# Kernel optimization log

Measured on AMD Instinct MI355X. Metric: run time of the kernel, lower is better.

Reference implementation:

```python
import jax, jax.numpy as jnp
import numpy as np
from jax import lax

K1, K2, DATA_RANGE = 0.01, 0.03, 1.0
MS_WEIGHTS = np.array([0.0448, 0.2856, 0.3001, 0.2363, 0.1333], dtype=np.float32)


def _gauss1d(size, sigma):
    coords = jnp.arange(size, dtype=jnp.float32) - size // 2
    g = jnp.exp(-(coords ** 2) / (2.0 * sigma ** 2))
    return g / jnp.sum(g)


def _gaussian_blur(x, win1d):
    # separable depthwise gaussian blur, VALID padding (matches pytorch-msssim)
    C = x.shape[1]
    size = win1d.shape[0]
    kh = jnp.tile(win1d.reshape(1, 1, size, 1), (C, 1, 1, 1))  # (C,1,k,1)
    kw = jnp.tile(win1d.reshape(1, 1, 1, size), (C, 1, 1, 1))  # (C,1,1,k)
    dn = ('NCHW', 'OIHW', 'NCHW')
    x = lax.conv_general_dilated(x, kh, (1, 1), 'VALID',
                                 dimension_numbers=dn, feature_group_count=C)
    x = lax.conv_general_dilated(x, kw, (1, 1), 'VALID',
                                 dimension_numbers=dn, feature_group_count=C)
    return x


def _ssim_per_channel(X, Y, win1d):
    C1 = (K1 * DATA_RANGE) ** 2
    C2 = (K2 * DATA_RANGE) ** 2
    mu1 = _gaussian_blur(X, win1d)
    mu2 = _gaussian_blur(Y, win1d)
    mu1_sq, mu2_sq, mu1_mu2 = mu1 * mu1, mu2 * mu2, mu1 * mu2
    sigma1_sq = _gaussian_blur(X * X, win1d) - mu1_sq
    sigma2_sq = _gaussian_blur(Y * Y, win1d) - mu2_sq
    sigma12 = _gaussian_blur(X * Y, win1d) - mu1_mu2
    cs_map = (2.0 * sigma12 + C2) / (sigma1_sq + sigma2_sq + C2)
    ssim_map = ((2.0 * mu1_mu2 + C1) / (mu1_sq + mu2_sq + C1)) * cs_map
    return ssim_map.mean(axis=(2, 3)), cs_map.mean(axis=(2, 3))  # (B,C) each


def _avg_pool2(x, ph, pw):
    # F.avg_pool2d(kernel=2, stride=2, padding=(ph,pw), count_include_pad=True)
    s = lax.reduce_window(x, 0.0, lax.add, (1, 1, 2, 2), (1, 1, 2, 2),
                          ((0, 0), (0, 0), (ph, ph), (pw, pw)))
    return s * 0.25


def _ms_ssim(gen, gt):
    weights = jnp.asarray(MS_WEIGHTS)
    win_size = 3 if gen.shape[3] < 256 else 11
    win1d = _gauss1d(win_size, 1.5)
    levels = weights.shape[0]
    mcs = []
    for i in range(levels):
        ssim_pc, cs = _ssim_per_channel(gen, gt, win1d)
        if i < levels - 1:
            mcs.append(jax.nn.relu(cs))
            ph, pw = gen.shape[2] % 2, gen.shape[3] % 2
            gen = _avg_pool2(gen, ph, pw)
            gt = _avg_pool2(gt, ph, pw)
    ssim_pc = jax.nn.relu(ssim_pc)
    mcs_and_ssim = jnp.stack(mcs + [ssim_pc], axis=0)  # (levels,B,C)
    ms_ssim_val = jnp.prod(mcs_and_ssim ** weights[:, None, None], axis=0)
    return ms_ssim_val.mean()


def setup_inputs() -> dict:
    key = jax.random.key(0)
    k1, k2 = jax.random.split(key)
    gen_frames = jax.random.uniform(k1, (16, 3, 512, 512), dtype=jnp.float32)
    gt_frames = jax.random.uniform(k2, (16, 3, 512, 512), dtype=jnp.float32)
    return {"gen_frames": gen_frames, "gt_frames": gt_frames}


def reference(gen_frames, gt_frames):
    return 1.0 - _ms_ssim(gen_frames, gt_frames)
```

## Files before the change

kernel.cpp:

```cpp
#include <hip/hip_runtime.h>


#define TW 32
#define TH 64
#define RPT 8
#define HALO 10
#define IW (TW + HALO)
#define IH (TH + HALO)
#define ISTR (IW + 1)

__device__ __constant__ float G11[11] = {
    0.001028380f, 0.007598758f, 0.036000773f, 0.109360680f, 0.213005529f,
    0.266011731f,
    0.213005529f, 0.109360680f, 0.036000773f, 0.007598758f, 0.001028380f
};

__device__ __forceinline__ float fastdiv(float a, float b) {
    float r = __builtin_amdgcn_rcpf(b);
    r = r * __builtin_fmaf(-b, r, 2.0f);
    return a * r;
}

#define HBLUR(ROW, SLOT) do {                                              \
    const float2* pxy_ = &sxy[(ROW) * ISTR + tx];                          \
    float bx_ = 0.f, by_ = 0.f, bxx_ = 0.f, byy_ = 0.f, bxy_ = 0.f;        \
    _Pragma("unroll")                                                      \
    for (int t_ = 0; t_ < 11; ++t_) {                                      \
        float w_  = G11[t_];                                               \
        float2 v_ = pxy_[t_];                                              \
        float wx_ = w_ * v_.x;                                             \
        float wy_ = w_ * v_.y;                                             \
        bx_  += wx_;                                                       \
        by_  += wy_;                                                       \
        bxx_ = __builtin_fmaf(wx_, v_.x, bxx_);                            \
        byy_ = __builtin_fmaf(wy_, v_.y, byy_);                            \
        bxy_ = __builtin_fmaf(wx_, v_.y, bxy_);                            \
    }                                                                      \
    rbx[(SLOT)] = bx_; rby[(SLOT)] = by_; rbxx[(SLOT)] = bxx_;             \
    rbyy[(SLOT)] = byy_; rbxy[(SLOT)] = bxy_;                              \
} while (0)

#define VTAP(I, T) do {                                                    \
    const float w_ = G11[(T)];                                             \
    m1  = __builtin_fmaf(w_, rbx [((I)+(T)) % 11], m1);                    \
    m2  = __builtin_fmaf(w_, rby [((I)+(T)) % 11], m2);                    \
    qxx = __builtin_fmaf(w_, rbxx[((I)+(T)) % 11], qxx);                   \
    qyy = __builtin_fmaf(w_, rbyy[((I)+(T)) % 11], qyy);                   \
    qxy = __builtin_fmaf(w_, rbxy[((I)+(T)) % 11], qxy);                   \
} while (0)

#define STEP(I) do {                                                       \
    HBLUR(g0 + 10 + (I), (10 + (I)) % 11);                                 \
    float m1 = 0.f, m2 = 0.f, qxx = 0.f, qyy = 0.f, qxy = 0.f;             \
    VTAP(I,0); VTAP(I,1); VTAP(I,2); VTAP(I,3); VTAP(I,4); VTAP(I,5);      \
    VTAP(I,6); VTAP(I,7); VTAP(I,8); VTAP(I,9); VTAP(I,10);                \
    if (colok && (oy + g0 + (I)) < Hs) {                                   \
        const float C1 = 0.0001f, C2 = 0.0009f;                            \
        float mu1s = m1 * m1, mu2s = m2 * m2, mu12 = m1 * m2;              \
        float s1  = qxx - mu1s;                                            \
        float s2  = qyy - mu2s;                                            \
        float s12 = qxy - mu12;                                            \
        float cs  = fastdiv(2.f * s12 + C2, s1 + s2 + C2);                 \
        float ss  = fastdiv((2.f * mu12 + C1) * cs, mu1s + mu2s + C1);     \
        ssum += ss;                                                        \
        csum += cs;                                                        \
    }                                                                      \
} while (0)

__global__ __launch_bounds__(256)
void ssim_level_kernel(const float* __restrict__ X, const float* __restrict__ Y,
                       int H, int W, int Hs, int Ws, float* __restrict__ acc,
                       float* __restrict__ Xo, float* __restrict__ Yo,
                       int Wp, int do_pool)
{
    __shared__ float2 sxy[IH * ISTR];
    __shared__ float red[2][4];

    const int bc  = blockIdx.z;
    const int ox  = blockIdx.x * TW;
    const int oy  = blockIdx.y * TH;
    const int tid = threadIdx.x;
    const size_t base = (size_t)bc * H * W;

    for (int p = tid; p < IH * 21; p += 256) {
        int r  = p / 21;
        int c2 = p - r * 21;
        int gr = oy + r;      if (gr > H - 1) gr = H - 1;
        int gc = ox + 2 * c2; if (gc > W - 2) gc = W - 2;
        size_t g = base + (size_t)gr * W + gc;
        float2 xv = *reinterpret_cast<const float2*>(X + g);
        float2 yv = *reinterpret_cast<const float2*>(Y + g);
        float2* dst = &sxy[r * ISTR + 2 * c2];
        dst[0] = make_float2(xv.x, yv.x);
        dst[1] = make_float2(xv.y, yv.y);
    }
    __syncthreads();

    const int tx = tid & 31;
    const int ty = tid >> 5;
    const int g0 = ty * RPT;

    float rbx[11], rby[11], rbxx[11], rbyy[11], rbxy[11];

    HBLUR(g0 + 0, 0); HBLUR(g0 + 1, 1); HBLUR(g0 + 2, 2); HBLUR(g0 + 3, 3);
    HBLUR(g0 + 4, 4); HBLUR(g0 + 5, 5); HBLUR(g0 + 6, 6); HBLUR(g0 + 7, 7);
    HBLUR(g0 + 8, 8); HBLUR(g0 + 9, 9);

    const bool colok = (ox + tx) < Ws;
    float ssum = 0.f, csum = 0.f;

    STEP(0); STEP(1); STEP(2); STEP(3);
    STEP(4); STEP(5); STEP(6); STEP(7);

    if (do_pool) {
        int i  = tid >> 3;
        int j0 = (tid & 7) * 2;
        const float2* r0 = &sxy[(2 * i)     * ISTR + 2 * j0];
        const float2* r1 = &sxy[(2 * i + 1) * ISTR + 2 * j0];
        float2 a0 = r0[0], a1 = r0[1], b0 = r1[0], b1 = r1[1];
        float2 c0 = r0[2], c1 = r0[3], d0 = r1[2], d1 = r1[3];
        float2 xo, yo;
        xo.x = 0.25f * (a0.x + a1.x + b0.x + b1.x);
        yo.x = 0.25f * (a0.y + a1.y + b0.y + b1.y);
        xo.y = 0.25f * (c0.x + c1.x + d0.x + d1.x);
        yo.y = 0.25f * (c0.y + c1.y + d0.y + d1.y);
        size_t po = (size_t)bc * Wp * Wp + (size_t)((oy >> 1) + i) * Wp + (ox >> 1) + j0;
        *reinterpret_cast<float2*>(Xo + po) = xo;
        *reinterpret_cast<float2*>(Yo + po) = yo;
    }

#pragma unroll
    for (int off = 32; off; off >>= 1) {
        ssum += __shfl_down(ssum, off);
        csum += __shfl_down(csum, off);
    }
    if ((tid & 63) == 0) {
        red[0][tid >> 6] = ssum;
        red[1][tid >> 6] = csum;
    }
    __syncthreads();
    if (tid == 0) {
        float s = red[0][0] + red[0][1] + red[0][2] + red[0][3];
        float c = red[1][0] + red[1][1] + red[1][2] + red[1][3];
        atomicAdd(&acc[bc * 2 + 0], s);
        atomicAdd(&acc[bc * 2 + 1], c);
    }
}

__launch_bounds__(64)
__global__ void finalize_kernel(const float* __restrict__ acc, float* __restrict__ out)
{
    const int lane = threadIdx.x;
    float prod = 0.f;
    if (lane < 48) {
        const float npix[5] = {252004.f, 60516.f, 13924.f, 2916.f, 484.f};
        const float wgt[5]  = {0.0448f, 0.2856f, 0.3001f, 0.2363f, 0.1333f};
        prod = 1.f;
#pragma unroll
        for (int l = 0; l < 5; ++l) {
            float v = (l < 4) ? acc[l * 96 + lane * 2 + 1] : acc[l * 96 + lane * 2 + 0];
            v = v / npix[l];
            v = fmaxf(v, 0.f);
            prod *= powf(v, wgt[l]);
        }
    }
#pragma unroll
    for (int off = 32; off; off >>= 1) prod += __shfl_down(prod, off);
    if (lane == 0) out[0] = 1.f - prod / 48.f;
}

extern "C" void kernel_launch(void* const* d_in, const int* in_sizes, int n_in,
                              void* d_out, int out_size, void* d_ws, size_t ws_size,
                              hipStream_t stream)
{
    const float* gen = (const float*)d_in[0];
    const float* gt  = (const float*)d_in[1];
    float* out = (float*)d_out;

    char* ws = (char*)d_ws;
    float* acc = (float*)ws;
    float* p   = (float*)(ws + 2048);
    float* g1 = p; p += (size_t)48 * 256 * 256;
    float* t1 = p; p += (size_t)48 * 256 * 256;
    float* g2 = p; p += (size_t)48 * 128 * 128;
    float* t2 = p; p += (size_t)48 * 128 * 128;
    float* g3 = p; p += (size_t)48 * 64 * 64;
    float* t3 = p; p += (size_t)48 * 64 * 64;
    float* g4 = p; p += (size_t)48 * 32 * 32;
    float* t4 = p; p += (size_t)48 * 32 * 32;

    hipMemsetAsync(acc, 0, 5 * 48 * 2 * sizeof(float), stream);

    auto launch_ssim = [&](const float* X, const float* Y, int H, int lvl,
                           float* Xo, float* Yo) {
        int Hs = H - 10;
        dim3 grid((Hs + TW - 1) / TW, (Hs + TH - 1) / TH, 48);
        ssim_level_kernel<<<grid, 256, 0, stream>>>(X, Y, H, H, Hs, Hs,
                                                    acc + lvl * 96,
                                                    Xo, Yo, H / 2, Xo != nullptr);
    };

    launch_ssim(gen, gt, 512, 0, g1, t1);
    launch_ssim(g1, t1, 256, 1, g2, t2);
    launch_ssim(g2, t2, 128, 2, g3, t3);
    launch_ssim(g3, t3, 64, 3, g4, t4);
    launch_ssim(g4, t4, 32, 4, nullptr, nullptr);
    finalize_kernel<<<1, 64, 0, stream>>>(acc, out);
}
```

Baseline: 283.7 us.

## Fuse last two pyramid levels into one per-image tail kernel

Levels 3 and 4 of the MS-SSIM pyramid now run in a single kernel with one block per image-channel. Each block loads the 64x64 plane into shared memory, computes level-3 SSIM, pools into shared memory and computes level-4 SSIM, so two launches and the global round trip of the level-4 images go away. The shared blur code was also refactored into a templated strip routine that keeps xx+yy as one summed term, removing one vertical-blur accumulator. The tail runs on only 48 blocks, so the GPU is mostly idle during it; the aim is to save launch overhead on these tiny levels.

```diff
diff --git a/kernel.cpp b/kernel.cpp
--- a/kernel.cpp
+++ b/kernel.cpp
@@ -1,13 +1,5 @@
 #include <hip/hip_runtime.h>
 
-
-#define TW 32
-#define TH 64
-#define RPT 8
-#define HALO 10
-#define IW (TW + HALO)
-#define IH (TH + HALO)
-#define ISTR (IW + 1)
 
 __device__ __constant__ float G11[11] = {
     0.001028380f, 0.007598758f, 0.036000773f, 0.109360680f, 0.213005529f,
@@ -21,51 +13,74 @@
     return a * r;
 }
 
-#define HBLUR(ROW, SLOT) do {                                              \
-    const float2* pxy_ = &sxy[(ROW) * ISTR + tx];                          \
-    float bx_ = 0.f, by_ = 0.f, bxx_ = 0.f, byy_ = 0.f, bxy_ = 0.f;        \
-    _Pragma("unroll")                                                      \
-    for (int t_ = 0; t_ < 11; ++t_) {                                      \
-        float w_  = G11[t_];                                               \
-        float2 v_ = pxy_[t_];                                              \
-        float wx_ = w_ * v_.x;                                             \
-        float wy_ = w_ * v_.y;                                             \
-        bx_  += wx_;                                                       \
-        by_  += wy_;                                                       \
-        bxx_ = __builtin_fmaf(wx_, v_.x, bxx_);                            \
-        byy_ = __builtin_fmaf(wy_, v_.y, byy_);                            \
-        bxy_ = __builtin_fmaf(wx_, v_.y, bxy_);                            \
-    }                                                                      \
-    rbx[(SLOT)] = bx_; rby[(SLOT)] = by_; rbxx[(SLOT)] = bxx_;             \
-    rbyy[(SLOT)] = byy_; rbxy[(SLOT)] = bxy_;                              \
+template<int NS, int STR>
+__device__ __forceinline__ void ssim_strip(const float2* __restrict__ tile,
+                                           int txr, int g0, int rowmax,
+                                           int nvalid, bool colok,
+                                           float& ssum, float& csum)
+{
+    float rbx[11], rby[11], rbss[11], rbxy[11];
+
+#define HB(K, SLOT) do {                                                    \
+    int r_ = g0 + (K); if (r_ > rowmax) r_ = rowmax;                        \
+    const float2* p_ = tile + r_ * STR + txr;                               \
+    float bx_=0.f, by_=0.f, bxx_=0.f, byy_=0.f, bxy_=0.f;                   \
+    _Pragma("unroll")                                                       \
+    for (int t_ = 0; t_ < 11; ++t_) {                                       \
+        float w_ = G11[t_];                                                 \
+        float2 v_ = p_[t_];                                                 \
+        float wx_ = w_ * v_.x;                                              \
+        float wy_ = w_ * v_.y;                                              \
+        bx_ += wx_; by_ += wy_;                                             \
+        bxx_ = __builtin_fmaf(wx_, v_.x, bxx_);                             \
+        byy_ = __builtin_fmaf(wy_, v_.y, byy_);                             \
+        bxy_ = __builtin_fmaf(wx_, v_.y, bxy_);                             \
+    }                                                                       \
+    rbx[(SLOT)] = bx_; rby[(SLOT)] = by_;                                   \
+    rbss[(SLOT)] = bxx_ + byy_; rbxy[(SLOT)] = bxy_;                        \
 } while (0)
 
-#define VTAP(I, T) do {                                                    \
-    const float w_ = G11[(T)];                                             \
-    m1  = __builtin_fmaf(w_, rbx [((I)+(T)) % 11], m1);                    \
-    m2  = __builtin_fmaf(w_, rby [((I)+(T)) % 11], m2);                    \
-    qxx = __builtin_fmaf(w_, rbxx[((I)+(T)) % 11], qxx);                   \
-    qyy = __builtin_fmaf(w_, rbyy[((I)+(T)) % 11], qyy);                   \
-    qxy = __builtin_fmaf(w_, rbxy[((I)+(T)) % 11], qxy);                   \
+#define VT(I, T) do {                                                       \
+    const float w_ = G11[(T)];                                              \
+    m1  = __builtin_fmaf(w_, rbx [((I)+(T)) % 11], m1);                     \
+    m2  = __builtin_fmaf(w_, rby [((I)+(T)) % 11], m2);                     \
+    qs  = __builtin_fmaf(w_, rbss[((I)+(T)) % 11], qs);                     \
+    qxy = __builtin_fmaf(w_, rbxy[((I)+(T)) % 11], qxy);                    \
 } while (0)
 
-#define STEP(I) do {                                                       \
-    HBLUR(g0 + 10 + (I), (10 + (I)) % 11);                                 \
-    float m1 = 0.f, m2 = 0.f, qxx = 0.f, qyy = 0.f, qxy = 0.f;             \
-    VTAP(I,0); VTAP(I,1); VTAP(I,2); VTAP(I,3); VTAP(I,4); VTAP(I,5);      \
-    VTAP(I,6); VTAP(I,7); VTAP(I,8); VTAP(I,9); VTAP(I,10);                \
-    if (colok && (oy + g0 + (I)) < Hs) {                                   \
-        const float C1 = 0.0001f, C2 = 0.0009f;                            \
-        float mu1s = m1 * m1, mu2s = m2 * m2, mu12 = m1 * m2;              \
-        float s1  = qxx - mu1s;                                            \
-        float s2  = qyy - mu2s;                                            \
-        float s12 = qxy - mu12;                                            \
-        float cs  = fastdiv(2.f * s12 + C2, s1 + s2 + C2);                 \
-        float ss  = fastdiv((2.f * mu12 + C1) * cs, mu1s + mu2s + C1);     \
-        ssum += ss;                                                        \
-        csum += cs;                                                        \
-    }                                                                      \
-} while (0)
+#define ST(I)                                                               \
+    if constexpr (NS > (I)) {                                               \
+        HB(10 + (I), (10 + (I)) % 11);                                      \
+        float m1=0.f, m2=0.f, qs=0.f, qxy=0.f;                              \
+        VT(I,0); VT(I,1); VT(I,2); VT(I,3); VT(I,4); VT(I,5);               \
+        VT(I,6); VT(I,7); VT(I,8); VT(I,9); VT(I,10);                       \
+        if (colok && (I) < nvalid) {                                        \
+            const float C1 = 0.0001f, C2 = 0.0009f;                         \
+            float mu1s = m1*m1, mu2s = m2*m2, mu12 = m1*m2;                 \
+            float s12  = qxy - mu12;                                        \
+            float s1s2 = qs - mu1s - mu2s;                                  \
+            float cs = fastdiv(2.f*s12 + C2, s1s2 + C2);                    \
+            float ss = fastdiv((2.f*mu12 + C1) * cs, mu1s + mu2s + C1);     \
+            ssum += ss; csum += cs;                                         \
+        }                                                                   \
+    }
+
+    HB(0,0); HB(1,1); HB(2,2); HB(3,3); HB(4,4);
+    HB(5,5); HB(6,6); HB(7,7); HB(8,8); HB(9,9);
+
+    ST(0) ST(1) ST(2) ST(3) ST(4) ST(5) ST(6) ST(7)
+    ST(8) ST(9) ST(10) ST(11) ST(12) ST(13) ST(14) ST(15)
+
+#undef HB
+#undef VT
+#undef ST
+}
+
+#define TW 32
+#define TH 64
+#define IW 42
+#define IH 74
+#define ISTR 43
 
 __global__ __launch_bounds__(256)
 void ssim_level_kernel(const float* __restrict__ X, const float* __restrict__ Y,
@@ -98,19 +113,11 @@
 
     const int tx = tid & 31;
     const int ty = tid >> 5;
-    const int g0 = ty * RPT;
-
-    float rbx[11], rby[11], rbxx[11], rbyy[11], rbxy[11];
-
-    HBLUR(g0 + 0, 0); HBLUR(g0 + 1, 1); HBLUR(g0 + 2, 2); HBLUR(g0 + 3, 3);
-    HBLUR(g0 + 4, 4); HBLUR(g0 + 5, 5); HBLUR(g0 + 6, 6); HBLUR(g0 + 7, 7);
-    HBLUR(g0 + 8, 8); HBLUR(g0 + 9, 9);
-
-    const bool colok = (ox + tx) < Ws;
+    const int g0 = ty * 8;
+
     float ssum = 0.f, csum = 0.f;
-
-    STEP(0); STEP(1); STEP(2); STEP(3);
-    STEP(4); STEP(5); STEP(6); STEP(7);
+    ssim_strip<8, ISTR>(sxy, tx, g0, IH - 1, Hs - oy - g0, (ox + tx) < Ws,
+                        ssum, csum);
 
     if (do_pool) {
         int i  = tid >> 3;
@@ -147,6 +154,74 @@
     }
 }
 
+#define L3STR 65
+#define L4STR 33
+
+__global__ __launch_bounds__(256)
+void ssim_tail_kernel(const float* __restrict__ X, const float* __restrict__ Y,
+                      float* __restrict__ acc)
+{
+    __shared__ float2 t3[64 * L3STR];
+    __shared__ float2 p4[32 * L4STR];
+    __shared__ float red[4][4];
+
+    const int bc  = blockIdx.x;
+    const int tid = threadIdx.x;
+    const size_t base = (size_t)bc * 64 * 64;
+
+    for (int p = tid; p < 64 * 32; p += 256) {
+        int r = p >> 5, c2 = p & 31;
+        size_t g = base + (size_t)r * 64 + 2 * c2;
+        float2 xv = *reinterpret_cast<const float2*>(X + g);
+        float2 yv = *reinterpret_cast<const float2*>(Y + g);
+        float2* dst = &t3[r * L3STR + 2 * c2];
+        dst[0] = make_float2(xv.x, yv.x);
+        dst[1] = make_float2(xv.y, yv.y);
+    }
+    __syncthreads();
+
+    float s3 = 0.f, c3 = 0.f;
+    {
+        int tx = tid & 63, ty = tid >> 6, g0 = ty * 14;
+        int txr = tx < 53 ? tx : 53;
+        ssim_strip<14, L3STR>(t3, txr, g0, 63, 54 - g0, tx < 54, s3, c3);
+    }
+
+    for (int p = tid; p < 32 * 32; p += 256) {
+        int r = p >> 5, c = p & 31;
+        const float2* r0 = &t3[(2 * r)     * L3STR + 2 * c];
+        const float2* r1 = &t3[(2 * r + 1) * L3STR + 2 * c];
+        float2 a = r0[0], b = r0[1], cc = r1[0], d = r1[1];
+        p4[r * L4STR + c] = make_float2(0.25f * (a.x + b.x + cc.x + d.x),
+                                        0.25f * (a.y + b.y + cc.y + d.y));
+    }
+    __syncthreads();
+
+    float s4 = 0.f, c4 = 0.f;
+    {
+        int tx = tid & 31, ty = tid >> 5, g0 = ty * 3;
+        int txr = tx < 21 ? tx : 21;
+        ssim_strip<3, L4STR>(p4, txr, g0, 31, 22 - g0, tx < 22, s4, c4);
+    }
+
+#pragma unroll
+    for (int off = 32; off; off >>= 1) {
+        s3 += __shfl_down(s3, off); c3 += __shfl_down(c3, off);
+        s4 += __shfl_down(s4, off); c4 += __shfl_down(c4, off);
+    }
+    if ((tid & 63) == 0) {
+        int w = tid >> 6;
+        red[0][w] = s3; red[1][w] = c3; red[2][w] = s4; red[3][w] = c4;
+    }
+    __syncthreads();
+    if (tid == 0) {
+        acc[3 * 96 + bc * 2 + 0] = red[0][0] + red[0][1] + red[0][2] + red[0][3];
+        acc[3 * 96 + bc * 2 + 1] = red[1][0] + red[1][1] + red[1][2] + red[1][3];
+        acc[4 * 96 + bc * 2 + 0] = red[2][0] + red[2][1] + red[2][2] + red[2][3];
+        acc[4 * 96 + bc * 2 + 1] = red[3][0] + red[3][1] + red[3][2] + red[3][3];
+    }
+}
+
 __launch_bounds__(64)
 __global__ void finalize_kernel(const float* __restrict__ acc, float* __restrict__ out)
 {
@@ -186,8 +261,6 @@
     float* t2 = p; p += (size_t)48 * 128 * 128;
     float* g3 = p; p += (size_t)48 * 64 * 64;
     float* t3 = p; p += (size_t)48 * 64 * 64;
-    float* g4 = p; p += (size_t)48 * 32 * 32;
-    float* t4 = p; p += (size_t)48 * 32 * 32;
 
     hipMemsetAsync(acc, 0, 5 * 48 * 2 * sizeof(float), stream);
 
@@ -197,13 +270,12 @@
         dim3 grid((Hs + TW - 1) / TW, (Hs + TH - 1) / TH, 48);
         ssim_level_kernel<<<grid, 256, 0, stream>>>(X, Y, H, H, Hs, Hs,
                                                     acc + lvl * 96,
-                                                    Xo, Yo, H / 2, Xo != nullptr);
+                                                    Xo, Yo, H / 2, 1);
     };
 
     launch_ssim(gen, gt, 512, 0, g1, t1);
     launch_ssim(g1, t1, 256, 1, g2, t2);
     launch_ssim(g2, t2, 128, 2, g3, t3);
-    launch_ssim(g3, t3, 64, 3, g4, t4);
-    launch_ssim(g4, t4, 32, 4, nullptr, nullptr);
+    ssim_tail_kernel<<<48, 256, 0, stream>>>(g3, t3, acc);
     finalize_kernel<<<1, 64, 0, stream>>>(acc, out);
 }
```

Result: no change. 278.9 us (-1.7%).
